# Optimization experiments

Hardware: AMD Instinct MI355X
Metric: run time of the kernel (lower is better)

The kernel has to match this reference:

```python
import math
import jax, jax.numpy as jnp
import numpy as np

N = 50000
C = 128      # in_channels == out_channels
H = 8        # nhead
D = C // H   # head_dim = 16
E = 800000


def _layernorm(x, g, b, eps=1e-5):
    mu = jnp.mean(x, axis=-1, keepdims=True)
    var = jnp.var(x, axis=-1, keepdims=True)
    return (x - mu) * jax.lax.rsqrt(var + eps) * g + b


def setup_inputs() -> dict:
    key = jax.random.key(0)
    ks = jax.random.split(key, 12)
    s = 1.0 / math.sqrt(C)          # ~xavier scale
    s4 = 1.0 / math.sqrt(4 * C)
    return {
        "x": jax.random.normal(ks[0], (N, C), dtype=jnp.float32),
        "edge_index": jax.random.randint(ks[1], (2, E), 0, N, dtype=jnp.int64),
        "Wq": jax.random.normal(ks[2], (C, C), dtype=jnp.float32) * s,
        "Wk": jax.random.normal(ks[3], (C, C), dtype=jnp.float32) * s,
        "Wv": jax.random.normal(ks[4], (C, C), dtype=jnp.float32) * s,
        "Wo": jax.random.normal(ks[5], (C, C), dtype=jnp.float32) * s,
        "bo": jnp.zeros((C,), dtype=jnp.float32),
        "Wf1": jax.random.normal(ks[6], (C, 4 * C), dtype=jnp.float32) * s,
        "bf1": jnp.zeros((4 * C,), dtype=jnp.float32),
        "Wf2": jax.random.normal(ks[7], (4 * C, C), dtype=jnp.float32) * s4,
        "bf2": jnp.zeros((C,), dtype=jnp.float32),
        "g1": jnp.ones((C,), dtype=jnp.float32),
        "b1": jnp.zeros((C,), dtype=jnp.float32),
        "g2": jnp.ones((C,), dtype=jnp.float32),
        "b2": jnp.zeros((C,), dtype=jnp.float32),
    }


def reference(x, edge_index, Wq, Wk, Wv, Wo, bo, Wf1, bf1, Wf2, bf2, g1, b1, g2, b2):
    n = x.shape[0]
    loops = jnp.arange(n, dtype=edge_index.dtype)
    row = jnp.concatenate([edge_index[0], loops])  # source nodes
    col = jnp.concatenate([edge_index[1], loops])  # destination nodes

    q = (x @ Wq).reshape(n, H, D)
    k = (x @ Wk).reshape(n, H, D)
    v = (x @ Wv).reshape(n, H, D)

    # edge-level attention scores [E+N, H]
    scores = jnp.einsum('ehd,ehd->eh', q[row], k[col]) / math.sqrt(D)
    smax = jax.ops.segment_max(scores, col, num_segments=n)  # every node has a self-loop
    exp = jnp.exp(scores - smax[col])
    ssum = jax.ops.segment_sum(exp, col, num_segments=n)
    alpha = exp / (ssum[col] + 1e-8)

    out = jax.ops.segment_sum(v[row] * alpha[..., None], col, num_segments=n)
    attn = out.reshape(n, C) @ Wo + bo

    residual = x  # input_proj is Identity (in_channels == out_channels)
    x1 = _layernorm(residual + attn, g1, b1)
    ffn = jax.nn.gelu(x1 @ Wf1 + bf1, approximate=False) @ Wf2 + bf2
    return _layernorm(x1 + ffn, g2, b2)
```

## Files before the change

kernel.cpp:

```cpp
#include <hip/hip_runtime.h>
#include <cmath>


typedef short bf16x8 __attribute__((ext_vector_type(8)));
typedef float f32x4 __attribute__((ext_vector_type(4)));
typedef unsigned int uint_as1 __attribute__((address_space(1)));
typedef unsigned int uint_as3 __attribute__((address_space(3)));

__device__ inline unsigned short f2bf(float f) {
    unsigned int u = __float_as_uint(f);
    u += 0x7fffu + ((u >> 16) & 1u);
    return (unsigned short)(u >> 16);
}
__device__ inline float bflo(unsigned int w) { return __uint_as_float(w << 16); }
__device__ inline float bfhi(unsigned int w) { return __uint_as_float(w & 0xffff0000u); }

__device__ inline void gload16(const unsigned short* g, unsigned short* l) {
    __builtin_amdgcn_global_load_lds((const uint_as1*)g, (uint_as3*)l, 16, 0, 0);
}


__global__ void k_zero(int* __restrict__ p, int n) {
    int i = blockIdx.x * 256 + threadIdx.x;
    if (i < n) p[i] = 0;
}

__global__ void k_count(const int* __restrict__ ei, int* __restrict__ counts,
                        int E, int N) {
    int e = blockIdx.x * 256 + threadIdx.x;
    if (e >= E + N) return;
    int col = (e < E) ? ei[E + e] : (e - E);
    atomicAdd(&counts[col], 1);
}

__global__ void k_scan1(const int* __restrict__ counts, int* __restrict__ incl,
                        int* __restrict__ bsums, int N) {
    __shared__ int s[256];
    int t = threadIdx.x, i = blockIdx.x * 256 + t;
    int v = (i < N) ? counts[i] : 0;
    s[t] = v; __syncthreads();
    for (int off = 1; off < 256; off <<= 1) {
        int add = (t >= off) ? s[t - off] : 0;
        __syncthreads();
        s[t] += add;
        __syncthreads();
    }
    if (i < N) incl[i] = s[t];
    if (t == 255) bsums[blockIdx.x] = s[255];
}

__global__ void k_scan2(const int* __restrict__ bsums, int* __restrict__ boffs, int NB) {
    __shared__ int s[256];
    int t = threadIdx.x;
    int v = (t < NB) ? bsums[t] : 0;
    s[t] = v; __syncthreads();
    for (int off = 1; off < 256; off <<= 1) {
        int add = (t >= off) ? s[t - off] : 0;
        __syncthreads();
        s[t] += add;
        __syncthreads();
    }
    if (t < NB) boffs[t] = s[t] - v;
}

__global__ void k_scan3(const int* __restrict__ incl, const int* __restrict__ counts,
                        const int* __restrict__ boffs, int* __restrict__ nstart,
                        int* __restrict__ cursor, int N) {
    int i = blockIdx.x * 256 + threadIdx.x;
    if (i >= N) return;
    int st = incl[i] - counts[i] + boffs[blockIdx.x];
    nstart[i] = st;
    cursor[i] = st;
}

__global__ void k_fill(const int* __restrict__ ei, int* __restrict__ cursor,
                       int* __restrict__ csr, int E, int N) {
    int e = blockIdx.x * 256 + threadIdx.x;
    if (e >= E + N) return;
    int row, col;
    if (e < E) { row = ei[e]; col = ei[E + e]; }
    else       { row = col = e - E; }
    int pos = atomicAdd(&cursor[col], 1);
    csr[pos] = row;
}


__global__ void k_cast(const float* __restrict__ x, unsigned short* __restrict__ xb,
                       int total4) {
    int i = blockIdx.x * 256 + threadIdx.x;
    if (i >= total4) return;
    float4 v = ((const float4*)x)[i];
    ushort4 o;
    o.x = f2bf(v.x); o.y = f2bf(v.y); o.z = f2bf(v.z); o.w = f2bf(v.w);
    ((ushort4*)xb)[i] = o;
}

__global__ void k_prep(const float* Wq, const float* Wk, const float* Wv, const float* Wo,
                       const float* Wf1, const float* Wf2,
                       unsigned short* Wqkvt, unsigned short* Wot,
                       unsigned short* Wf1t, unsigned short* Wf2t) {
    int z = blockIdx.y;
    const float* in; unsigned short* out; int K, Co;
    switch (z) {
        case 0: in = Wq;  out = Wqkvt;          K = 128; Co = 128; break;
        case 1: in = Wk;  out = Wqkvt + 16384;  K = 128; Co = 128; break;
        case 2: in = Wv;  out = Wqkvt + 32768;  K = 128; Co = 128; break;
        case 3: in = Wo;  out = Wot;            K = 128; Co = 128; break;
        case 4: in = Wf1; out = Wf1t;           K = 128; Co = 512; break;
        default: in = Wf2; out = Wf2t;          K = 512; Co = 128; break;
    }
    int idx = blockIdx.x * 256 + threadIdx.x;
    if (idx >= K * Co) return;
    int k = idx / Co, c = idx % Co;
    out[c * K + k] = f2bf(in[idx]);
}


template <int EPI>
__global__ __launch_bounds__(256) void k_gemm_big(
    const unsigned short* __restrict__ A, const unsigned short* __restrict__ Bt,
    const float* __restrict__ bias, const float* __restrict__ resid,
    const float* __restrict__ g, const float* __restrict__ b,
    float* __restrict__ outf, unsigned short* __restrict__ outb,
    int M, int K, int Cout) {
    __shared__ unsigned short As[128 * 64];
    __shared__ unsigned short Bs[128 * 64];
    __shared__ float pSum[2][128];
    __shared__ float pSq[2][128];

    int tid = threadIdx.x;
    int wid = tid >> 6, lane = tid & 63;
    int quad = lane >> 4, l16 = lane & 15;
    int wr = wid >> 1, wc = wid & 1;
    int m0 = blockIdx.x * 128;
    int n0 = blockIdx.y * 128;

    int srow = tid >> 3;
    int gch = (tid & 7) ^ (srow & 7);
    const unsigned short* gA[4];
    const unsigned short* gB[4];
#pragma unroll
    for (int j = 0; j < 4; ++j) {
        int ra = m0 + j * 32 + srow; if (ra > M - 1) ra = M - 1;
        gA[j] = A + (size_t)ra * K + gch * 8;
        gB[j] = Bt + (size_t)(n0 + j * 32 + srow) * K + gch * 8;
    }

    f32x4 acc[4][4];
#pragma unroll
    for (int i = 0; i < 4; ++i)
#pragma unroll
        for (int j = 0; j < 4; ++j) acc[i][j] = {0.f, 0.f, 0.f, 0.f};

    int KT = K >> 6;
    for (int kt = 0; kt < KT; ++kt) {
        int ko = kt * 64;
#pragma unroll
        for (int j = 0; j < 4; ++j) {
            gload16(gA[j] + ko, As + j * 2048 + tid * 8);
            gload16(gB[j] + ko, Bs + j * 2048 + tid * 8);
        }
        __syncthreads();
#pragma unroll
        for (int s = 0; s < 2; ++s) {
            int swz = ((s * 4 + quad) ^ (l16 & 7)) * 8;
            bf16x8 af[4], bfr[4];
#pragma unroll
            for (int t4 = 0; t4 < 4; ++t4) {
                af[t4]  = *(const bf16x8*)&As[(wr * 64 + t4 * 16 + l16) * 64 + swz];
                bfr[t4] = *(const bf16x8*)&Bs[(wc * 64 + t4 * 16 + l16) * 64 + swz];
            }
#pragma unroll
            for (int ti = 0; ti < 4; ++ti)
#pragma unroll
                for (int tj = 0; tj < 4; ++tj)
                    acc[ti][tj] = __builtin_amdgcn_mfma_f32_16x16x32_bf16(
                        af[ti], bfr[tj], acc[ti][tj], 0, 0, 0);
        }
        __syncthreads();
    }

    if constexpr (EPI != 2) {
#pragma unroll
        for (int ti = 0; ti < 4; ++ti)
#pragma unroll
            for (int tj = 0; tj < 4; ++tj) {
                int col = n0 + wc * 64 + tj * 16 + l16;
#pragma unroll
                for (int r = 0; r < 4; ++r) {
                    int row = m0 + wr * 64 + ti * 16 + quad * 4 + r;
                    if (row >= M) continue;
                    float v = acc[ti][tj][r];
                    if constexpr (EPI == 1) {
                        float gg = v + bias[col];
                        v = 0.5f * gg * (1.f + erff(gg * 0.70710678118f));
                    }
                    outb[(size_t)row * Cout + col] = f2bf(v);
                }
            }
    } else {
        float bi[4], gv[4], bv[4];
#pragma unroll
        for (int tj = 0; tj < 4; ++tj) {
            int col = wc * 64 + tj * 16 + l16;
            bi[tj] = bias[col]; gv[tj] = g[col]; bv[tj] = b[col];
        }
#pragma unroll
        for (int ti = 0; ti < 4; ++ti)
#pragma unroll
            for (int tj = 0; tj < 4; ++tj) {
                int col = wc * 64 + tj * 16 + l16;
#pragma unroll
                for (int r = 0; r < 4; ++r) {
                    int row = m0 + wr * 64 + ti * 16 + quad * 4 + r;
                    float rv = (row < M) ? resid[(size_t)row * 128 + col] : 0.f;
                    acc[ti][tj][r] += bi[tj] + rv;
                }
            }
#pragma unroll
        for (int ti = 0; ti < 4; ++ti)
#pragma unroll
            for (int r = 0; r < 4; ++r) {
                float s = acc[ti][0][r] + acc[ti][1][r] + acc[ti][2][r] + acc[ti][3][r];
                float q = acc[ti][0][r] * acc[ti][0][r] + acc[ti][1][r] * acc[ti][1][r]
                        + acc[ti][2][r] * acc[ti][2][r] + acc[ti][3][r] * acc[ti][3][r];
                s += __shfl_xor(s, 1); q += __shfl_xor(q, 1);
                s += __shfl_xor(s, 2); q += __shfl_xor(q, 2);
                s += __shfl_xor(s, 4); q += __shfl_xor(q, 4);
                s += __shfl_xor(s, 8); q += __shfl_xor(q, 8);
                if (l16 == 0) {
                    int lr = wr * 64 + ti * 16 + quad * 4 + r;
                    pSum[wc][lr] = s; pSq[wc][lr] = q;
                }
            }
        __syncthreads();
        if (tid < 128) {
            float s = pSum[0][tid] + pSum[1][tid];
            float q = pSq[0][tid] + pSq[1][tid];
            float mean = s * 0.0078125f;
            float var = q * 0.0078125f - mean * mean;
            pSum[0][tid] = mean;
            pSq[0][tid] = rsqrtf(var + 1e-5f);
        }
        __syncthreads();
#pragma unroll
        for (int ti = 0; ti < 4; ++ti)
#pragma unroll
            for (int r = 0; r < 4; ++r) {
                int lr = wr * 64 + ti * 16 + quad * 4 + r;
                int row = m0 + lr;
                if (row >= M) continue;
                float mean = pSum[0][lr], rs = pSq[0][lr];
#pragma unroll
                for (int tj = 0; tj < 4; ++tj) {
                    int col = wc * 64 + tj * 16 + l16;
                    float y = (acc[ti][tj][r] - mean) * rs * gv[tj] + bv[tj];
                    if (outf) outf[(size_t)row * 128 + col] = y;
                    if (outb) outb[(size_t)row * 128 + col] = f2bf(y);
                }
            }
    }
}


__global__ __launch_bounds__(256) void k_attn(
    const unsigned int* __restrict__ qkv, const int* __restrict__ nstart,
    const int* __restrict__ counts, const int* __restrict__ csr,
    unsigned int* __restrict__ ob, int N) {
    int j = blockIdx.x * 4 + (threadIdx.x >> 6);
    if (j >= N) return;
    int l = threadIdx.x & 63;

    unsigned int kw = qkv[(size_t)j * 192 + 64 + l];
    float kx = bflo(kw), ky = bfhi(kw);

    int start = nstart[j], cnt = counts[j];
    float m = -3.0e38f, lsum = 0.f, a0 = 0.f, a1 = 0.f;
    int i = 0;
    for (; i + 4 <= cnt; i += 4) {
        int r0 = csr[start + i + 0], r1 = csr[start + i + 1];
        int r2 = csr[start + i + 2], r3 = csr[start + i + 3];
        unsigned int qw0 = qkv[(size_t)r0 * 192 + l];
        unsigned int qw1 = qkv[(size_t)r1 * 192 + l];
        unsigned int qw2 = qkv[(size_t)r2 * 192 + l];
        unsigned int qw3 = qkv[(size_t)r3 * 192 + l];
        unsigned int vw0 = qkv[(size_t)r0 * 192 + 128 + l];
        unsigned int vw1 = qkv[(size_t)r1 * 192 + 128 + l];
        unsigned int vw2 = qkv[(size_t)r2 * 192 + 128 + l];
        unsigned int vw3 = qkv[(size_t)r3 * 192 + 128 + l];

        float p0 = fmaf(bflo(qw0), kx, bfhi(qw0) * ky);
        float p1 = fmaf(bflo(qw1), kx, bfhi(qw1) * ky);
        float p2 = fmaf(bflo(qw2), kx, bfhi(qw2) * ky);
        float p3 = fmaf(bflo(qw3), kx, bfhi(qw3) * ky);
        p0 += __shfl_xor(p0, 1); p1 += __shfl_xor(p1, 1);
        p2 += __shfl_xor(p2, 1); p3 += __shfl_xor(p3, 1);
        p0 += __shfl_xor(p0, 2); p1 += __shfl_xor(p1, 2);
        p2 += __shfl_xor(p2, 2); p3 += __shfl_xor(p3, 2);
        p0 += __shfl_xor(p0, 4); p1 += __shfl_xor(p1, 4);
        p2 += __shfl_xor(p2, 4); p3 += __shfl_xor(p3, 4);
        float s0 = p0 * 0.25f, s1 = p1 * 0.25f, s2 = p2 * 0.25f, s3 = p3 * 0.25f;

        float mn = fmaxf(fmaxf(fmaxf(s0, s1), fmaxf(s2, s3)), m);
        float scale = __expf(m - mn);
        float e0 = __expf(s0 - mn), e1 = __expf(s1 - mn);
        float e2 = __expf(s2 - mn), e3 = __expf(s3 - mn);
        lsum = lsum * scale + ((e0 + e1) + (e2 + e3));
        a0 = a0 * scale + e0 * bflo(vw0) + e1 * bflo(vw1) + e2 * bflo(vw2) + e3 * bflo(vw3);
        a1 = a1 * scale + e0 * bfhi(vw0) + e1 * bfhi(vw1) + e2 * bfhi(vw2) + e3 * bfhi(vw3);
        m = mn;
    }
    for (; i < cnt; ++i) {
        int r = csr[start + i];
        unsigned int qw = qkv[(size_t)r * 192 + l];
        unsigned int vw = qkv[(size_t)r * 192 + 128 + l];
        float p = fmaf(bflo(qw), kx, bfhi(qw) * ky);
        p += __shfl_xor(p, 1);
        p += __shfl_xor(p, 2);
        p += __shfl_xor(p, 4);
        float sc = p * 0.25f;
        float mn = fmaxf(m, sc);
        float scale = __expf(m - mn);
        float e = __expf(sc - mn);
        lsum = lsum * scale + e;
        a0 = a0 * scale + e * bflo(vw);
        a1 = a1 * scale + e * bfhi(vw);
        m = mn;
    }
    float inv = 1.f / (lsum + 1e-8f);
    unsigned int w = ((unsigned int)f2bf(a1 * inv) << 16) | (unsigned int)f2bf(a0 * inv);
    ob[(size_t)j * 64 + l] = w;
}


extern "C" void kernel_launch(void* const* d_in, const int* in_sizes, int n_in,
                              void* d_out, int out_size, void* d_ws, size_t ws_size,
                              hipStream_t stream) {
    const float* x   = (const float*)d_in[0];
    const int* ei    = (const int*)d_in[1];
    const float* Wq  = (const float*)d_in[2];
    const float* Wk  = (const float*)d_in[3];
    const float* Wv  = (const float*)d_in[4];
    const float* Wo  = (const float*)d_in[5];
    const float* bo  = (const float*)d_in[6];
    const float* Wf1 = (const float*)d_in[7];
    const float* bf1 = (const float*)d_in[8];
    const float* Wf2 = (const float*)d_in[9];
    const float* bf2 = (const float*)d_in[10];
    const float* g1  = (const float*)d_in[11];
    const float* b1  = (const float*)d_in[12];
    const float* g2  = (const float*)d_in[13];
    const float* b2  = (const float*)d_in[14];

    int N = in_sizes[0] / 128;
    int E = in_sizes[1] / 2;
    int N2 = ((N + 127) / 128) * 128;
    int NE = E + N;

    char* p = (char*)d_ws;
    auto alloc = [&](size_t bytes) -> char* {
        char* r = p;
        p += (bytes + 255) & ~(size_t)255;
        return r;
    };
    unsigned short* qkv = (unsigned short*)alloc((size_t)N2 * 512 * 2);
    unsigned short* ob  = qkv + (size_t)N2 * 384;
    unsigned short* hb  = qkv;
    unsigned short* x1b = (unsigned short*)alloc((size_t)N2 * 128 * 2);
    unsigned short* xb  = x1b;
    float* x1f          = (float*)alloc((size_t)N2 * 128 * 4);
    unsigned short* Wqkvt = (unsigned short*)alloc(3 * 128 * 128 * 2);
    unsigned short* Wot   = (unsigned short*)alloc(128 * 128 * 2);
    unsigned short* Wf1t  = (unsigned short*)alloc(512 * 128 * 2);
    unsigned short* Wf2t  = (unsigned short*)alloc(128 * 512 * 2);
    int* counts = (int*)alloc((size_t)N * 4);
    int* incl   = (int*)alloc((size_t)N * 4);
    int* nstart = (int*)alloc((size_t)N * 4);
    int* cursor = (int*)alloc((size_t)N * 4);
    int* bsums  = (int*)alloc(1024 * 4);
    int* boffs  = (int*)alloc(1024 * 4);
    int* csr    = (int*)alloc((size_t)NE * 4);

    int NB = (N + 255) / 256;
    int M128 = (N + 127) / 128;

    k_zero<<<NB, 256, 0, stream>>>(counts, N);
    k_count<<<(NE + 255) / 256, 256, 0, stream>>>(ei, counts, E, N);
    k_scan1<<<NB, 256, 0, stream>>>(counts, incl, bsums, N);
    k_scan2<<<1, 256, 0, stream>>>(bsums, boffs, NB);
    k_scan3<<<NB, 256, 0, stream>>>(incl, counts, boffs, nstart, cursor, N);
    k_fill<<<(NE + 255) / 256, 256, 0, stream>>>(ei, cursor, csr, E, N);

    k_cast<<<((N * 128 / 4) + 255) / 256, 256, 0, stream>>>(x, xb, N * 128 / 4);
    k_prep<<<dim3(256, 6), 256, 0, stream>>>(Wq, Wk, Wv, Wo, Wf1, Wf2,
                                             Wqkvt, Wot, Wf1t, Wf2t);

    k_gemm_big<0><<<dim3(M128, 3), 256, 0, stream>>>(
        xb, Wqkvt, nullptr, nullptr, nullptr, nullptr, nullptr, qkv, N, 128, 384);

    k_attn<<<(N + 3) / 4, 256, 0, stream>>>((const unsigned int*)qkv, nstart,
                                            counts, csr, (unsigned int*)ob, N);

    k_gemm_big<2><<<dim3(M128, 1), 256, 0, stream>>>(
        ob, Wot, bo, x, g1, b1, x1f, x1b, N, 128, 128);

    k_gemm_big<1><<<dim3(M128, 4), 256, 0, stream>>>(
        x1b, Wf1t, bf1, nullptr, nullptr, nullptr, nullptr, hb, N, 128, 512);

    k_gemm_big<2><<<dim3(M128, 1), 256, 0, stream>>>(
        hb, Wf2t, bf2, x1f, g2, b2, (float*)d_out, nullptr, N, 512, 128);
}
```

Baseline: 387.3 us.

## Restructure GEMMs to keep whole-K weight tile in LDS, stream A into registers

The GEMM kernel now loads the entire K-extent of the weight tile into LDS once, with a swizzled layout, and reads A fragments straight from global memory into registers. This removes the per-K-step LDS staging of A and the barriers between steps. The final FFN GEMM uses 512-thread blocks covering 256 rows, with A loads double-buffered against the MFMA chunks. Exact erf GELU is replaced by a polynomial approximation (Abramowitz-Stegun) using a fast reciprocal and exp, which adds a small accuracy risk. LDS usage grows for K=512 (128 KB), which may limit occupancy.

```diff
diff --git a/kernel.cpp b/kernel.cpp
--- a/kernel.cpp
+++ b/kernel.cpp
@@ -17,6 +17,20 @@
 
 __device__ inline void gload16(const unsigned short* g, unsigned short* l) {
     __builtin_amdgcn_global_load_lds((const uint_as1*)g, (uint_as3*)l, 16, 0, 0);
+}
+
+__device__ inline float gelu_f(float x) {
+    float ax = fabsf(x) * 0.70710678118f;
+    float t = __builtin_amdgcn_rcpf(fmaf(0.3275911f, ax, 1.0f));
+    float p = fmaf(1.061405429f, t, -1.453152027f);
+    p = fmaf(p, t, 1.421413741f);
+    p = fmaf(p, t, -0.284496736f);
+    p = fmaf(p, t, 0.254829592f);
+    p = p * t;
+    float e = __expf(-ax * ax);
+    float pe = p * e;
+    float w = (x >= 0.f) ? (2.0f - pe) : pe;
+    return 0.5f * x * w;
 }
 
 
@@ -116,35 +130,56 @@
 }
 
 
-template <int EPI>
-__global__ __launch_bounds__(256) void k_gemm_big(
+template <int EPI, int KS, int WR>
+__global__ __launch_bounds__(WR * 128, WR == 2 ? 3 : 2) void k_gemm(
     const unsigned short* __restrict__ A, const unsigned short* __restrict__ Bt,
     const float* __restrict__ bias, const float* __restrict__ resid,
     const float* __restrict__ g, const float* __restrict__ b,
     float* __restrict__ outf, unsigned short* __restrict__ outb,
-    int M, int K, int Cout) {
-    __shared__ unsigned short As[128 * 64];
-    __shared__ unsigned short Bs[128 * 64];
-    __shared__ float pSum[2][128];
-    __shared__ float pSq[2][128];
+    int M, int Cout) {
+    constexpr int K = KS * 32;
+    constexpr int NT = WR * 128;
+    constexpr int CPR = K / 8;
+    constexpr int RPI = NT / CPR;
+    constexpr int NITER = 128 / RPI;
+    __shared__ unsigned short Bs[128 * K];
 
     int tid = threadIdx.x;
     int wid = tid >> 6, lane = tid & 63;
     int quad = lane >> 4, l16 = lane & 15;
     int wr = wid >> 1, wc = wid & 1;
-    int m0 = blockIdx.x * 128;
+    int m0 = blockIdx.x * (WR * 64);
     int n0 = blockIdx.y * 128;
 
-    int srow = tid >> 3;
-    int gch = (tid & 7) ^ (srow & 7);
-    const unsigned short* gA[4];
-    const unsigned short* gB[4];
-#pragma unroll
-    for (int j = 0; j < 4; ++j) {
-        int ra = m0 + j * 32 + srow; if (ra > M - 1) ra = M - 1;
-        gA[j] = A + (size_t)ra * K + gch * 8;
-        gB[j] = Bt + (size_t)(n0 + j * 32 + srow) * K + gch * 8;
-    }
+    const unsigned short* Arow[4];
+#pragma unroll
+    for (int ti = 0; ti < 4; ++ti) {
+        int row = m0 + wr * 64 + ti * 16 + l16;
+        if (row > M - 1) row = M - 1;
+        Arow[ti] = A + (size_t)row * K + quad * 8;
+    }
+
+#define LOADA(buf, kc)                                                        \
+    _Pragma("unroll") for (int ti_ = 0; ti_ < 4; ++ti_)                       \
+        _Pragma("unroll") for (int j_ = 0; j_ < 4; ++j_)                      \
+            buf[ti_][j_] = *(const bf16x8*)(Arow[ti_] + ((kc) + j_) * 32);
+
+    bf16x8 a0[4][4];
+    LOADA(a0, 0);
+    bf16x8 a1[4][4];
+    if constexpr (KS > 4) { LOADA(a1, 4); }
+
+    {
+        int srow = tid / CPR;
+        int c = tid % CPR;
+        int gc = (c & ~7) | ((c & 7) ^ (srow & 7));
+        const unsigned short* src = Bt + (size_t)(n0 + srow) * K + gc * 8;
+        unsigned short* dst = Bs + tid * 8;
+#pragma unroll
+        for (int j = 0; j < NITER; ++j)
+            gload16(src + (size_t)j * RPI * K, dst + (size_t)j * RPI * K);
+    }
+    __syncthreads();
 
     f32x4 acc[4][4];
 #pragma unroll
@@ -152,33 +187,31 @@
 #pragma unroll
         for (int j = 0; j < 4; ++j) acc[i][j] = {0.f, 0.f, 0.f, 0.f};
 
-    int KT = K >> 6;
-    for (int kt = 0; kt < KT; ++kt) {
-        int ko = kt * 64;
-#pragma unroll
-        for (int j = 0; j < 4; ++j) {
-            gload16(gA[j] + ko, As + j * 2048 + tid * 8);
-            gload16(gB[j] + ko, Bs + j * 2048 + tid * 8);
-        }
-        __syncthreads();
-#pragma unroll
-        for (int s = 0; s < 2; ++s) {
-            int swz = ((s * 4 + quad) ^ (l16 & 7)) * 8;
-            bf16x8 af[4], bfr[4];
-#pragma unroll
-            for (int t4 = 0; t4 < 4; ++t4) {
-                af[t4]  = *(const bf16x8*)&As[(wr * 64 + t4 * 16 + l16) * 64 + swz];
-                bfr[t4] = *(const bf16x8*)&Bs[(wc * 64 + t4 * 16 + l16) * 64 + swz];
-            }
-#pragma unroll
-            for (int ti = 0; ti < 4; ++ti)
-#pragma unroll
-                for (int tj = 0; tj < 4; ++tj)
-                    acc[ti][tj] = __builtin_amdgcn_mfma_f32_16x16x32_bf16(
-                        af[ti], bfr[tj], acc[ti][tj], 0, 0, 0);
-        }
-        __syncthreads();
-    }
+#define KCHUNK(buf, kc)                                                       \
+    _Pragma("unroll") for (int ks_ = 0; ks_ < 4; ++ks_) {                     \
+        bf16x8 bfr[4];                                                        \
+        _Pragma("unroll") for (int tj_ = 0; tj_ < 4; ++tj_) {                 \
+            int nr = wc * 64 + tj_ * 16 + l16;                                \
+            int cidx = ((kc) + ks_) * 4 + quad;                               \
+            int slot = (cidx & ~7) | ((cidx & 7) ^ (nr & 7));                 \
+            bfr[tj_] = *(const bf16x8*)&Bs[nr * K + slot * 8];                \
+        }                                                                     \
+        _Pragma("unroll") for (int ti_ = 0; ti_ < 4; ++ti_)                   \
+            _Pragma("unroll") for (int tj_ = 0; tj_ < 4; ++tj_)               \
+                acc[ti_][tj_] = __builtin_amdgcn_mfma_f32_16x16x32_bf16(      \
+                    buf[ti_][ks_], bfr[tj_], acc[ti_][tj_], 0, 0, 0);         \
+    }
+
+    KCHUNK(a0, 0);
+    if constexpr (KS > 4) {
+        LOADA(a0, 8);
+        KCHUNK(a1, 4);
+        LOADA(a1, 12);
+        KCHUNK(a0, 8);
+        KCHUNK(a1, 12);
+    }
+#undef LOADA
+#undef KCHUNK
 
     if constexpr (EPI != 2) {
 #pragma unroll
@@ -191,14 +224,13 @@
                     int row = m0 + wr * 64 + ti * 16 + quad * 4 + r;
                     if (row >= M) continue;
                     float v = acc[ti][tj][r];
-                    if constexpr (EPI == 1) {
-                        float gg = v + bias[col];
-                        v = 0.5f * gg * (1.f + erff(gg * 0.70710678118f));
-                    }
+                    if constexpr (EPI == 1) v = gelu_f(v + bias[col]);
                     outb[(size_t)row * Cout + col] = f2bf(v);
                 }
             }
     } else {
+        __shared__ float pSum[2][WR * 64];
+        __shared__ float pSq[2][WR * 64];
         float bi[4], gv[4], bv[4];
 #pragma unroll
         for (int tj = 0; tj < 4; ++tj) {
@@ -234,7 +266,7 @@
                 }
             }
         __syncthreads();
-        if (tid < 128) {
+        if (tid < WR * 64) {
             float s = pSum[0][tid] + pSum[1][tid];
             float q = pSq[0][tid] + pSq[1][tid];
             float mean = s * 0.0078125f;
@@ -383,6 +415,7 @@
 
     int NB = (N + 255) / 256;
     int M128 = (N + 127) / 128;
+    int M256 = (N + 255) / 256;
 
     k_zero<<<NB, 256, 0, stream>>>(counts, N);
     k_count<<<(NE + 255) / 256, 256, 0, stream>>>(ei, counts, E, N);
@@ -395,18 +428,18 @@
     k_prep<<<dim3(256, 6), 256, 0, stream>>>(Wq, Wk, Wv, Wo, Wf1, Wf2,
                                              Wqkvt, Wot, Wf1t, Wf2t);
 
-    k_gemm_big<0><<<dim3(M128, 3), 256, 0, stream>>>(
-        xb, Wqkvt, nullptr, nullptr, nullptr, nullptr, nullptr, qkv, N, 128, 384);
+    k_gemm<0, 4, 2><<<dim3(M128, 3), 256, 0, stream>>>(
+        xb, Wqkvt, nullptr, nullptr, nullptr, nullptr, nullptr, qkv, N, 384);
 
     k_attn<<<(N + 3) / 4, 256, 0, stream>>>((const unsigned int*)qkv, nstart,
                                             counts, csr, (unsigned int*)ob, N);
 
-    k_gemm_big<2><<<dim3(M128, 1), 256, 0, stream>>>(
-        ob, Wot, bo, x, g1, b1, x1f, x1b, N, 128, 128);
-
-    k_gemm_big<1><<<dim3(M128, 4), 256, 0, stream>>>(
-        x1b, Wf1t, bf1, nullptr, nullptr, nullptr, nullptr, hb, N, 128, 512);
-
-    k_gemm_big<2><<<dim3(M128, 1), 256, 0, stream>>>(
-        hb, Wf2t, bf2, x1f, g2, b2, (float*)d_out, nullptr, N, 512, 128);
-}
+    k_gemm<2, 4, 2><<<dim3(M128, 1), 256, 0, stream>>>(
+        ob, Wot, bo, x, g1, b1, x1f, x1b, N, 128);
+
+    k_gemm<1, 4, 2><<<dim3(M128, 4), 256, 0, stream>>>(
+        x1b, Wf1t, bf1, nullptr, nullptr, nullptr, nullptr, hb, N, 512);
+
+    k_gemm<2, 16, 4><<<dim3(M256, 1), 512, 0, stream>>>(
+        hb, Wf2t, bf2, x1f, g2, b2, (float*)d_out, nullptr, N, 128);
+}
```

Result: no change. 384.2 us (-0.8%).
